# Optimization experiments

Hardware: AMD Instinct MI355X
Metric: run time of the kernel (lower is better)

The kernel has to match this reference:

```python
import jax, jax.numpy as jnp
import numpy as np

NUM_CLUSTERS = 16
HIDDEN = 1024
BOTTLENECK = 128
N_TOKENS = 65536


def setup_inputs() -> dict:
    key = jax.random.key(0)
    k_h, k_ids, k_w1, k_b1, k_w2, k_b2 = jax.random.split(key, 6)
    h = jax.random.normal(k_h, (N_TOKENS, HIDDEN), dtype=jnp.float32)
    cluster_ids = jax.random.randint(k_ids, (N_TOKENS,), 0, NUM_CLUSTERS)
    # Stacked per-cluster adapter params (torch Linear: y = x @ W.T + b; we store
    # already-transposed weights so forward is x @ W1[c]).
    s1 = 1.0 / np.sqrt(HIDDEN)
    s2 = 1.0 / np.sqrt(BOTTLENECK)
    W1 = jax.random.uniform(k_w1, (NUM_CLUSTERS, HIDDEN, BOTTLENECK), jnp.float32, -s1, s1)
    b1 = jax.random.uniform(k_b1, (NUM_CLUSTERS, BOTTLENECK), jnp.float32, -s1, s1)
    # Original inits these to zero; use small random values so grads are non-trivial.
    W2 = jax.random.uniform(k_w2, (NUM_CLUSTERS, BOTTLENECK, HIDDEN), jnp.float32, -s2, s2) * 0.02
    b2 = jax.random.uniform(k_b2, (NUM_CLUSTERS, HIDDEN), jnp.float32, -s2, s2) * 0.02
    return {"h": h, "cluster_ids": cluster_ids, "W1": W1, "b1": b1, "W2": W2, "b2": b2}


def reference(h, cluster_ids, W1, b1, W2, b2):
    # h: [N, H]; cluster_ids: [N]; W1: [K, H, B]; b1: [K, B]; W2: [K, B, H]; b2: [K, H]
    # out[n] = h[n] + adapter_{cluster_ids[n]}(h[n])
    K = W1.shape[0]
    out = jnp.zeros_like(h)
    for c in range(K):  # fixed small expert count; select per-token result via where
        mid = jax.nn.gelu(h @ W1[c] + b1[c], approximate=False)  # [N, B]
        y = h + mid @ W2[c] + b2[c]                               # [N, H]
        out = jnp.where((cluster_ids == c)[:, None], y, out)
    return out
```

## Files before the change

kernel.cpp:

```cpp
#include <hip/hip_runtime.h>
#include <hip/hip_bf16.h>
#include <math.h>

#define NUM_CLUSTERS 16
#define HIDDEN 1024
#define BOT 128
#define NTOK 65536

typedef __attribute__((ext_vector_type(8))) short bf16x8;
typedef __attribute__((ext_vector_type(4))) float f32x4;

typedef __attribute__((address_space(3))) unsigned int lds_u32;
typedef const __attribute__((address_space(1))) unsigned int glb_u32;

__device__ __forceinline__ void gload16(const void* g, void* l) {
  __builtin_amdgcn_global_load_lds((glb_u32*)g, (lds_u32*)l, 16, 0, 0);
}

__device__ __forceinline__ unsigned short f2bf(float x) {
  union { float f; unsigned u; } v; v.f = x;
  unsigned r = v.u + 0x7fffu + ((v.u >> 16) & 1u);
  return (unsigned short)(r >> 16);
}

__device__ __forceinline__ bf16x8 pack8(float4 a, float4 b) {
  bf16x8 r;
  r[0] = (short)f2bf(a.x); r[1] = (short)f2bf(a.y);
  r[2] = (short)f2bf(a.z); r[3] = (short)f2bf(a.w);
  r[4] = (short)f2bf(b.x); r[5] = (short)f2bf(b.y);
  r[6] = (short)f2bf(b.z); r[7] = (short)f2bf(b.w);
  return r;
}

#define SWZS(row, sidx) ((sidx) ^ (((row) & 7) << 3))
#define SW4(row, fidx) ((fidx) ^ (((row) & 7) << 2))

#define SCB() __builtin_amdgcn_sched_barrier(0)
#define VMW(n)                                          \
  do {                                                  \
    SCB();                                              \
    asm volatile("s_waitcnt vmcnt(" #n ")" ::: "memory"); \
    SCB();                                              \
  } while (0)
#define SBAR()                                  \
  do {                                          \
    SCB();                                      \
    __builtin_amdgcn_s_barrier();               \
    SCB();                                      \
  } while (0)
#define LGKM0() asm volatile("s_waitcnt lgkmcnt(0)" ::: "memory")

__device__ __forceinline__ int xcd_swz(int bid, int nwg) {
  const int nx = 8;
  int q = nwg / nx, r = nwg % nx;
  int xcd = bid % nx, idx = bid / nx;
  int b = (xcd < r) ? xcd * (q + 1) : r * (q + 1) + (xcd - r) * q;
  return b + idx;
}


__global__ void k_zero(int* p) {
  if (threadIdx.x < 64) p[threadIdx.x] = 0;
}

__global__ void k_hist(const int* __restrict__ ids, int* __restrict__ counts) {
  __shared__ int lh[NUM_CLUSTERS];
  if (threadIdx.x < NUM_CLUSTERS) lh[threadIdx.x] = 0;
  __syncthreads();
  int i = blockIdx.x * blockDim.x + threadIdx.x;
  int stride = gridDim.x * blockDim.x;
  for (; i < NTOK; i += stride) atomicAdd(&lh[ids[i]], 1);
  __syncthreads();
  if (threadIdx.x < NUM_CLUSTERS) atomicAdd(&counts[threadIdx.x], lh[threadIdx.x]);
}

__global__ void k_scan(const int* __restrict__ counts, int* __restrict__ offsets,
                       int* __restrict__ cursor) {
  if (threadIdx.x == 0 && blockIdx.x == 0) {
    int s = 0;
    for (int c = 0; c < NUM_CLUSTERS; ++c) {
      offsets[c] = s; cursor[c] = s; s += counts[c];
    }
    offsets[NUM_CLUSTERS] = s;
  }
}

__global__ void k_scatter(const int* __restrict__ ids, int* cursor,
                          int* __restrict__ perm) {
  __shared__ int lh[NUM_CLUSTERS], lbase[NUM_CLUSTERS];
  const int tid = threadIdx.x;
  if (tid < NUM_CLUSTERS) lh[tid] = 0;
  __syncthreads();
  const int i = blockIdx.x * 256 + tid;
  const int cc = ids[i];
  const int r = atomicAdd(&lh[cc], 1);
  __syncthreads();
  if (tid < NUM_CLUSTERS) lbase[tid] = atomicAdd(&cursor[tid], lh[tid]);
  __syncthreads();
  perm[lbase[cc] + r] = i;
}

__global__ void k_w1til(const float* __restrict__ W1, unsigned short* __restrict__ outw) {
  const int id = blockIdx.x * 256 + threadIdx.x;
  const int c  = id >> 14;
  const int ks = (id >> 10) & 15;
  const int q  = id & 1023;
  const int o  = q << 4;
  const int row = o >> 7;
  const int lb  = (o & 127) ^ ((row & 7) << 4);
  const int k0  = ks * 64 + (lb >> 1);
  const float* src = W1 + ((size_t)c * HIDDEN + k0) * BOT + row;
  unsigned short v[8];
  #pragma unroll
  for (int j = 0; j < 8; ++j) v[j] = f2bf(src[(size_t)j * BOT]);
  *(uint4*)((char*)outw + ((size_t)(c * 16 + ks)) * 16384 + o) = *(const uint4*)v;
}

__global__ void k_w2lin(const float* __restrict__ W2, unsigned short* __restrict__ outw) {
  const int id = blockIdx.x * 256 + threadIdx.x;
  const int c   = id >> 14;
  const int rem = id & 16383;
  const int fg  = rem >> 6;
  const int l   = rem & 63;
  const int nc  = fg >> 4, kk = (fg >> 2) & 3, nf = fg & 3;
  const int n   = nc * 64 + nf * 16 + (l & 15);
  const int k0  = kk * 32 + (l >> 4) * 8;
  const float* src = W2 + ((size_t)c * BOT + k0) * HIDDEN + n;
  unsigned short v[8];
  #pragma unroll
  for (int j = 0; j < 8; ++j) v[j] = f2bf(src[(size_t)j * HIDDEN]);
  *(uint4*)(outw + (size_t)id * 8) = *(const uint4*)v;
}

__global__ void k_w2til(const float* __restrict__ W2, unsigned short* __restrict__ outw) {
  const int id = blockIdx.x * 256 + threadIdx.x;
  const int c  = id >> 14;
  const int nc = (id >> 10) & 15;
  const int q  = id & 1023;
  const int o  = q << 4;
  const int row = o >> 8;
  const int lb  = (o & 255) ^ ((row & 7) << 4);
  const int b0  = lb >> 1;
  const int n   = nc * 64 + row;
  const float* src = W2 + ((size_t)c * BOT + b0) * HIDDEN + n;
  unsigned short v[8];
  #pragma unroll
  for (int j = 0; j < 8; ++j) v[j] = f2bf(src[(size_t)j * HIDDEN]);
  *(uint4*)((char*)outw + ((size_t)(c * 16 + nc)) * 16384 + o) = *(const uint4*)v;
}

__device__ __forceinline__ bool locate(const int* offsets, int bid, int TMv,
                                       int& c, int& base, int& nvalid) {
  int t = bid;
  for (c = 0; c < NUM_CLUSTERS; ++c) {
    int cnt = offsets[c + 1] - offsets[c];
    int nt = (cnt + TMv - 1) / TMv;
    if (t < nt) {
      base = offsets[c] + t * TMv;
      nvalid = min(TMv, offsets[c + 1] - base);
      return true;
    }
    t -= nt;
  }
  return false;
}

__global__ __launch_bounds__(512, 6) void k_gemm1(
    const float* __restrict__ h, const float* __restrict__ b1g,
    const unsigned short* __restrict__ W1til, const int* __restrict__ offsets,
    const int* __restrict__ perm, unsigned short* __restrict__ midg) {

  __shared__ __align__(16) unsigned short sA[2][4096];
  __shared__ __align__(16) unsigned short sB[2][8192];
  __shared__ int sTok[64];

  const int tid = threadIdx.x;
  const int l = tid & 63, w = tid >> 6;
  const int lr = l & 15, lg = l >> 4;
  const int wr = w >> 2, wc = w & 3;
  const int row = tid >> 3, o8 = tid & 7;

  const int nwg = NTOK / 64 + NUM_CLUSTERS;
  int c, base, nvalid;
  if (!locate(offsets, xcd_swz(blockIdx.x, nwg), 64, c, base, nvalid)) return;

  if (tid < 64) sTok[tid] = perm[base + min(tid, nvalid - 1)];
  LGKM0();
  SBAR();

  const unsigned short* w1base = W1til + (size_t)c * 16 * 8192;
  const float* hrow = h + (long)sTok[row] * HIDDEN + o8 * 8;

  float4 vaA[2], vaB[2];
  vaA[0] = *(const float4*)(hrow);       vaA[1] = *(const float4*)(hrow + 4);
  SCB();
  gload16(w1base + tid * 8, &sB[0][tid * 8]);
  gload16(w1base + 4096 + tid * 8, &sB[0][4096 + tid * 8]);
  SCB();
  vaB[0] = *(const float4*)(hrow + 64);  vaB[1] = *(const float4*)(hrow + 68);
  SCB();
  *(bf16x8*)&sA[0][SWZS(row, row * 64 + o8 * 8)] = pack8(vaA[0], vaA[1]);
  LGKM0();
  VMW(2);
  SBAR();

  f32x4 acc[2][2];
  #pragma unroll
  for (int i = 0; i < 2; ++i)
    #pragma unroll
    for (int j = 0; j < 2; ++j) { f32x4 z = {0.f, 0.f, 0.f, 0.f}; acc[i][j] = z; }

#define G1_MFMA(CUR)                                                          \
  do {                                                                        \
    _Pragma("unroll")                                                         \
    for (int kk = 0; kk < 2; ++kk) {                                          \
      bf16x8 af[2], bfr[2];                                                   \
      _Pragma("unroll")                                                       \
      for (int mf = 0; mf < 2; ++mf) {                                        \
        const int m = wr * 32 + mf * 16 + lr;                                 \
        af[mf] = *(const bf16x8*)&sA[CUR][SWZS(m, m * 64 + kk * 32 + lg * 8)];\
      }                                                                       \
      _Pragma("unroll")                                                       \
      for (int nf = 0; nf < 2; ++nf) {                                        \
        const int rn = wc * 32 + nf * 16 + lr;                                \
        bfr[nf] = *(const bf16x8*)&sB[CUR][SWZS(rn, rn * 64 + kk * 32 + lg * 8)]; \
      }                                                                       \
      _Pragma("unroll")                                                       \
      for (int mf = 0; mf < 2; ++mf)                                          \
        _Pragma("unroll")                                                     \
        for (int nf = 0; nf < 2; ++nf)                                        \
          acc[mf][nf] = __builtin_amdgcn_mfma_f32_16x16x32_bf16(              \
              af[mf], bfr[nf], acc[mf][nf], 0, 0, 0);                         \
    }                                                                         \
  } while (0)

  #pragma unroll
  for (int t = 0; t < 16; ++t) {
    const int cur = t & 1;
    if (t < 15) {
      const unsigned short* w1s = w1base + (t + 1) * 8192;
      gload16(w1s + tid * 8, &sB[cur ^ 1][tid * 8]);
      gload16(w1s + 4096 + tid * 8, &sB[cur ^ 1][4096 + tid * 8]);
      SCB();
    }
    if (t < 14) {
      if (t & 1) {
        vaB[0] = *(const float4*)(hrow + (t + 2) * 64);
        vaB[1] = *(const float4*)(hrow + (t + 2) * 64 + 4);
      } else {
        vaA[0] = *(const float4*)(hrow + (t + 2) * 64);
        vaA[1] = *(const float4*)(hrow + (t + 2) * 64 + 4);
      }
      SCB();
    }
    G1_MFMA(cur);
    if (t < 15) {
      const float4* src = ((t + 1) & 1) ? vaB : vaA;
      *(bf16x8*)&sA[cur ^ 1][SWZS(row, row * 64 + o8 * 8)] = pack8(src[0], src[1]);
      if (t < 14) { VMW(2); } else { VMW(0); }
      LGKM0();
      SBAR();
    }
  }
#undef G1_MFMA

  float b1v[2];
  #pragma unroll
  for (int nf = 0; nf < 2; ++nf) b1v[nf] = b1g[c * BOT + wc * 32 + nf * 16 + lr];
  #pragma unroll
  for (int mf = 0; mf < 2; ++mf) {
    #pragma unroll
    for (int nf = 0; nf < 2; ++nf) {
      #pragma unroll
      for (int r = 0; r < 4; ++r) {
        float x = acc[mf][nf][r] + b1v[nf];
        float g = 0.5f * x * (1.0f + erff(x * 0.70710678118654752f));
        const int m = wr * 32 + mf * 16 + lg * 4 + r;
        if (m < nvalid) {
          const int n = wc * 32 + nf * 16 + lr;
          midg[(size_t)(base + m) * BOT + n] = f2bf(g);
        }
      }
    }
  }
}


__global__ __launch_bounds__(512, 6) void k_gemm2(
    const float* __restrict__ h, const float* __restrict__ b2g,
    const unsigned short* __restrict__ W2lin, const int* __restrict__ offsets,
    const int* __restrict__ perm, const unsigned short* __restrict__ midg,
    float* __restrict__ out) {

  __shared__ __align__(16) unsigned short sB[2][8192];
  __shared__ __align__(16) float sOut[8 * 512];
  __shared__ int sTok[64];

  const int tid = threadIdx.x;
  const int l = tid & 63, w = tid >> 6;
  const int lr = l & 15, lg = l >> 4;
  const int wrow = (w & 3) * 16;
  const int ch = w >> 2;

  const int nwg = NTOK / 64 + NUM_CLUSTERS;
  int c, base, nvalid;
  if (!locate(offsets, xcd_swz(blockIdx.x, nwg), 64, c, base, nvalid)) return;

  if (tid < 64) sTok[tid] = perm[base + min(tid, nvalid - 1)];
  __syncthreads();

  const unsigned short* wlin = W2lin + (size_t)c * 131072;

  const long amrow = (long)(base + min(wrow + lr, nvalid - 1)) * BOT;
  bf16x8 ma[4];
  #pragma unroll
  for (int kk = 0; kk < 4; ++kk)
    ma[kk] = *(const bf16x8*)(midg + amrow + kk * 32 + lg * 8);

  const int er = l >> 2, ecq = l & 3;
  const long etok = (long)sTok[wrow + er] * HIDDEN;
  const float* hrow = h + etok;
  float* orow = out + etok;
  float* sW = sOut + w * 512;
  const float* b2c = b2g + c * HIDDEN;
  const int ecol = ch * 32 + ecq * 8;

  gload16(wlin + tid * 8, &sB[0][tid * 8]);
  gload16(wlin + 4096 + tid * 8, &sB[0][4096 + tid * 8]);
  VMW(0);
  SBAR();

  for (int nc = 0; nc < 16; ++nc) {
    const int cur = nc & 1;
    float4 hv0 = *(const float4*)(hrow + nc * 64 + ecol);
    float4 hv1 = *(const float4*)(hrow + nc * 64 + ecol + 4);
    float4 bv0 = *(const float4*)(b2c + nc * 64 + ecol);
    float4 bv1 = *(const float4*)(b2c + nc * 64 + ecol + 4);
    SCB();
    if (nc < 15) {
      const unsigned short* ws2 = wlin + (nc + 1) * 8192;
      gload16(ws2 + tid * 8, &sB[cur ^ 1][tid * 8]);
      gload16(ws2 + 4096 + tid * 8, &sB[cur ^ 1][4096 + tid * 8]);
      SCB();
    }

    f32x4 acc[2];
    { f32x4 z = {0.f, 0.f, 0.f, 0.f}; acc[0] = z; acc[1] = z; }
    #pragma unroll
    for (int kk = 0; kk < 4; ++kk) {
      #pragma unroll
      for (int nf = 0; nf < 2; ++nf) {
        const bf16x8 bf =
            *(const bf16x8*)&sB[cur][(kk * 4 + ch * 2 + nf) * 512 + l * 8];
        acc[nf] = __builtin_amdgcn_mfma_f32_16x16x32_bf16(ma[kk], bf, acc[nf], 0, 0, 0);
      }
    }

    #pragma unroll
    for (int nf = 0; nf < 2; ++nf) {
      #pragma unroll
      for (int r = 0; r < 4; ++r) {
        const int m = lg * 4 + r;
        const int n = nf * 16 + lr;
        sW[(m * 32 + n) ^ ((m & 7) << 2)] = acc[nf][r];
      }
    }
    {
      const int fb = er * 32 + ecq * 8;
      const float4 y0 = *(const float4*)&sW[(fb) ^ ((er & 7) << 2)];
      const float4 y1 = *(const float4*)&sW[(fb + 4) ^ ((er & 7) << 2)];
      float4 o0, o1;
      o0.x = y0.x + hv0.x + bv0.x; o0.y = y0.y + hv0.y + bv0.y;
      o0.z = y0.z + hv0.z + bv0.z; o0.w = y0.w + hv0.w + bv0.w;
      o1.x = y1.x + hv1.x + bv1.x; o1.y = y1.y + hv1.y + bv1.y;
      o1.z = y1.z + hv1.z + bv1.z; o1.w = y1.w + hv1.w + bv1.w;
      *(float4*)(orow + nc * 64 + ecol)     = o0;
      *(float4*)(orow + nc * 64 + ecol + 4) = o1;
    }
    if (nc < 15) {
      VMW(2);
      SBAR();
    }
  }
}

#define FSWZ(row, sidx) ((sidx) ^ (((row) & 7) << 3))

__global__ __launch_bounds__(256, 2) void k_fused(
    const float* __restrict__ h, const float* __restrict__ b1g,
    const float* __restrict__ b2g, const unsigned short* __restrict__ W1til,
    const unsigned short* __restrict__ W2til, const int* __restrict__ offsets,
    const int* __restrict__ perm, float* __restrict__ out) {

  __shared__ __align__(16) unsigned short sAB[16384];
  __shared__ __align__(16) unsigned short sMid[16384];
  __shared__ int sTok[128];

  const int tid = threadIdx.x;
  const int l = tid & 63, w = tid >> 6;
  const int wr = w >> 1, wc = w & 1;
  const int lr = l & 15, lg = l >> 4;

  int c, base, nvalid;
  if (!locate(offsets, blockIdx.x, 128, c, base, nvalid)) return;

  if (tid < 128) sTok[tid] = perm[base + min(tid, nvalid - 1)];
  __syncthreads();

  const unsigned short* w1base = W1til + (size_t)c * 16 * 8192;
  const unsigned short* w2base = W2til + (size_t)c * 16 * 8192;

  const int arow = tid >> 1, ahalf = tid & 1;
  const long htok = (long)sTok[arow] * HIDDEN;

  f32x4 acc[4][4];
  #pragma unroll
  for (int i = 0; i < 4; ++i)
    #pragma unroll
    for (int j = 0; j < 4; ++j) { f32x4 z = {0.f, 0.f, 0.f, 0.f}; acc[i][j] = z; }

  for (int ks = 0; ks < 16; ++ks) {
    __syncthreads();
    const unsigned short* w1s = w1base + ks * 8192;
    #pragma unroll
    for (int j = 0; j < 4; ++j)
      gload16(w1s + j * 2048 + tid * 8, &sAB[8192 + j * 2048 + tid * 8]);
    {
      const float* hp = h + htok + ks * 64 + ahalf * 32;
      float4 v0 = *(const float4*)(hp + 0),  v1 = *(const float4*)(hp + 4);
      float4 v2 = *(const float4*)(hp + 8),  v3 = *(const float4*)(hp + 12);
      float4 v4 = *(const float4*)(hp + 16), v5 = *(const float4*)(hp + 20);
      float4 v6 = *(const float4*)(hp + 24), v7 = *(const float4*)(hp + 28);
      const int sb = arow * 64 + ahalf * 32;
      *(bf16x8*)&sAB[FSWZ(arow, sb + 0)]  = pack8(v0, v1);
      *(bf16x8*)&sAB[FSWZ(arow, sb + 8)]  = pack8(v2, v3);
      *(bf16x8*)&sAB[FSWZ(arow, sb + 16)] = pack8(v4, v5);
      *(bf16x8*)&sAB[FSWZ(arow, sb + 24)] = pack8(v6, v7);
    }
    __syncthreads();
    #pragma unroll
    for (int kk = 0; kk < 2; ++kk) {
      bf16x8 af[4], bfr[4];
      #pragma unroll
      for (int mf = 0; mf < 4; ++mf) {
        const int rw = wr * 64 + mf * 16 + lr;
        af[mf] = *(const bf16x8*)&sAB[FSWZ(rw, rw * 64 + kk * 32 + lg * 8)];
      }
      #pragma unroll
      for (int nf = 0; nf < 4; ++nf) {
        const int rn = wc * 64 + nf * 16 + lr;
        bfr[nf] = *(const bf16x8*)&sAB[8192 + FSWZ(rn, rn * 64 + kk * 32 + lg * 8)];
      }
      #pragma unroll
      for (int mf = 0; mf < 4; ++mf)
        #pragma unroll
        for (int nf = 0; nf < 4; ++nf)
          acc[mf][nf] = __builtin_amdgcn_mfma_f32_16x16x32_bf16(af[mf], bfr[nf], acc[mf][nf], 0, 0, 0);
    }
  }

  float b1v[4];
  #pragma unroll
  for (int nf = 0; nf < 4; ++nf) b1v[nf] = b1g[c * BOT + wc * 64 + nf * 16 + lr];
  #pragma unroll
  for (int mf = 0; mf < 4; ++mf)
    #pragma unroll
    for (int nf = 0; nf < 4; ++nf)
      #pragma unroll
      for (int r = 0; r < 4; ++r) {
        float x = acc[mf][nf][r] + b1v[nf];
        float g = 0.5f * x * (1.0f + erff(x * 0.70710678118654752f));
        const int m = wr * 64 + mf * 16 + lg * 4 + r;
        const int n = wc * 64 + nf * 16 + lr;
        sMid[FSWZ(m, m * 128 + n)] = f2bf(g);
      }

  for (int nc = 0; nc < 16; ++nc) {
    __syncthreads();
    #pragma unroll
    for (int j = 0; j < 4; ++j)
      gload16(w2base + nc * 8192 + j * 2048 + tid * 8, &sAB[j * 2048 + tid * 8]);
    __syncthreads();

    f32x4 a2[4][2];
    #pragma unroll
    for (int i = 0; i < 4; ++i)
      #pragma unroll
      for (int j = 0; j < 2; ++j) { f32x4 z = {0.f, 0.f, 0.f, 0.f}; a2[i][j] = z; }

    #pragma unroll
    for (int kk = 0; kk < 4; ++kk) {
      bf16x8 af[4], bfr[2];
      #pragma unroll
      for (int mf = 0; mf < 4; ++mf) {
        const int m = wr * 64 + mf * 16 + lr;
        af[mf] = *(const bf16x8*)&sMid[FSWZ(m, m * 128 + kk * 32 + lg * 8)];
      }
      #pragma unroll
      for (int nf = 0; nf < 2; ++nf) {
        const int rn = wc * 32 + nf * 16 + lr;
        bfr[nf] = *(const bf16x8*)&sAB[FSWZ(rn, rn * 128 + kk * 32 + lg * 8)];
      }
      #pragma unroll
      for (int mf = 0; mf < 4; ++mf)
        #pragma unroll
        for (int nf = 0; nf < 2; ++nf)
          a2[mf][nf] = __builtin_amdgcn_mfma_f32_16x16x32_bf16(af[mf], bfr[nf], a2[mf][nf], 0, 0, 0);
    }

    #pragma unroll
    for (int nf = 0; nf < 2; ++nf) {
      const int nn = nc * 64 + wc * 32 + nf * 16 + lr;
      const float b2v = b2g[c * HIDDEN + nn];
      #pragma unroll
      for (int mf = 0; mf < 4; ++mf)
        #pragma unroll
        for (int r = 0; r < 4; ++r) {
          const int m = wr * 64 + mf * 16 + lg * 4 + r;
          if (m < nvalid) {
            const long tk = (long)sTok[m] * HIDDEN;
            out[tk + nn] = h[tk + nn] + a2[mf][nf][r] + b2v;
          }
        }
    }
  }
}

extern "C" void kernel_launch(void* const* d_in, const int* in_sizes, int n_in,
                              void* d_out, int out_size, void* d_ws, size_t ws_size,
                              hipStream_t stream) {
  const float* h   = (const float*)d_in[0];
  const int*   ids = (const int*)d_in[1];
  const float* W1  = (const float*)d_in[2];
  const float* b1  = (const float*)d_in[3];
  const float* W2  = (const float*)d_in[4];
  const float* b2  = (const float*)d_in[5];
  float* out = (float*)d_out;

  char* ws = (char*)d_ws;
  int* counts  = (int*)ws;
  int* cursor  = (int*)(ws + 64);
  int* offsets = (int*)(ws + 128);
  int* perm    = (int*)(ws + 256);
  unsigned short* W1til = (unsigned short*)(ws + 262400);
  unsigned short* W2buf = W1til + (size_t)16 * 16 * 8192;
  unsigned short* midg  = W2buf + (size_t)16 * 16 * 8192;
  const size_t need = 262400 + 2 * (size_t)16 * 16 * 8192 * 2 +
                      (size_t)NTOK * BOT * 2;

  k_zero<<<1, 64, 0, stream>>>(counts);
  k_hist<<<256, 256, 0, stream>>>(ids, counts);
  k_scan<<<1, 64, 0, stream>>>(counts, offsets, cursor);
  k_scatter<<<NTOK / 256, 256, 0, stream>>>(ids, cursor, perm);
  k_w1til<<<1024, 256, 0, stream>>>(W1, W1til);

  if (ws_size >= need) {
    k_w2lin<<<1024, 256, 0, stream>>>(W2, W2buf);
    const int nwg = NTOK / 64 + NUM_CLUSTERS;
    k_gemm1<<<nwg, 512, 0, stream>>>(h, b1, W1til, offsets, perm, midg);
    k_gemm2<<<nwg, 512, 0, stream>>>(h, b2, W2buf, offsets, perm, midg, out);
  } else {
    k_w2til<<<1024, 256, 0, stream>>>(W2, W2buf);
    k_fused<<<NTOK / 128 + NUM_CLUSTERS, 256, 0, stream>>>(
        h, b1, b2, W1til, W2buf, offsets, perm, out);
  }
}
```

Measured before the change: 268.5 us.

## Fuse adapter GEMM1 and GEMM2 into one kernel with mid kept in LDS

Merges the two grouped GEMM kernels into one, so the GELU bottleneck activations are written to LDS instead of a global bf16 buffer and read back directly as MFMA A-operands. This removes the global round trip of the mid tensor and one kernel launch. The epilogue now writes output straight from MFMA accumulator layout with scalar loads and stores instead of staging through LDS for float4 stores, which may make h loads and output stores less coalesced. Out-of-range rows in partial tiles also write duplicates of the last valid token.

```diff
diff --git a/kernel.cpp b/kernel.cpp
--- a/kernel.cpp
+++ b/kernel.cpp
@@ -33,7 +33,6 @@
 }
 
 #define SWZS(row, sidx) ((sidx) ^ (((row) & 7) << 3))
-#define SW4(row, fidx) ((fidx) ^ (((row) & 7) << 2))
 
 #define SCB() __builtin_amdgcn_sched_barrier(0)
 #define VMW(n)                                          \
@@ -165,10 +164,12 @@
   return false;
 }
 
-__global__ __launch_bounds__(512, 6) void k_gemm1(
+
+__global__ __launch_bounds__(512, 6) void k_fuse(
     const float* __restrict__ h, const float* __restrict__ b1g,
-    const unsigned short* __restrict__ W1til, const int* __restrict__ offsets,
-    const int* __restrict__ perm, unsigned short* __restrict__ midg) {
+    const float* __restrict__ b2g, const unsigned short* __restrict__ W1til,
+    const unsigned short* __restrict__ W2lin, const int* __restrict__ offsets,
+    const int* __restrict__ perm, float* __restrict__ out) {
 
   __shared__ __align__(16) unsigned short sA[2][4096];
   __shared__ __align__(16) unsigned short sB[2][8192];
@@ -189,6 +190,7 @@
   SBAR();
 
   const unsigned short* w1base = W1til + (size_t)c * 16 * 8192;
+  const unsigned short* wlin   = W2lin + (size_t)c * 131072;
   const float* hrow = h + (long)sTok[row] * HIDDEN + o8 * 8;
 
   float4 vaA[2], vaB[2];
@@ -264,78 +266,67 @@
   }
 #undef G1_MFMA
 
-  float b1v[2];
-  #pragma unroll
-  for (int nf = 0; nf < 2; ++nf) b1v[nf] = b1g[c * BOT + wc * 32 + nf * 16 + lr];
-  #pragma unroll
-  for (int mf = 0; mf < 2; ++mf) {
-    #pragma unroll
-    for (int nf = 0; nf < 2; ++nf) {
-      #pragma unroll
-      for (int r = 0; r < 4; ++r) {
-        float x = acc[mf][nf][r] + b1v[nf];
-        float g = 0.5f * x * (1.0f + erff(x * 0.70710678118654752f));
-        const int m = wr * 32 + mf * 16 + lg * 4 + r;
-        if (m < nvalid) {
+  unsigned short* sMid = &sA[0][0];
+  gload16(wlin + tid * 8, &sB[0][tid * 8]);
+  gload16(wlin + 4096 + tid * 8, &sB[0][4096 + tid * 8]);
+  SCB();
+  SBAR();
+
+  {
+    float b1v[2];
+    #pragma unroll
+    for (int nf = 0; nf < 2; ++nf) b1v[nf] = b1g[c * BOT + wc * 32 + nf * 16 + lr];
+    #pragma unroll
+    for (int mf = 0; mf < 2; ++mf) {
+      #pragma unroll
+      for (int nf = 0; nf < 2; ++nf) {
+        #pragma unroll
+        for (int r = 0; r < 4; ++r) {
+          float x = acc[mf][nf][r] + b1v[nf];
+          float g = 0.5f * x * (1.0f + erff(x * 0.70710678118654752f));
+          const int m = wr * 32 + mf * 16 + lg * 4 + r;
           const int n = wc * 32 + nf * 16 + lr;
-          midg[(size_t)(base + m) * BOT + n] = f2bf(g);
+          sMid[SWZS(m, m * 128 + n)] = f2bf(g);
         }
       }
     }
   }
-}
-
-
-__global__ __launch_bounds__(512, 6) void k_gemm2(
-    const float* __restrict__ h, const float* __restrict__ b2g,
-    const unsigned short* __restrict__ W2lin, const int* __restrict__ offsets,
-    const int* __restrict__ perm, const unsigned short* __restrict__ midg,
-    float* __restrict__ out) {
-
-  __shared__ __align__(16) unsigned short sB[2][8192];
-  __shared__ __align__(16) float sOut[8 * 512];
-  __shared__ int sTok[64];
-
-  const int tid = threadIdx.x;
-  const int l = tid & 63, w = tid >> 6;
-  const int lr = l & 15, lg = l >> 4;
+  LGKM0();
+  VMW(0);
+  SBAR();
+
   const int wrow = (w & 3) * 16;
   const int ch = w >> 2;
 
-  const int nwg = NTOK / 64 + NUM_CLUSTERS;
-  int c, base, nvalid;
-  if (!locate(offsets, xcd_swz(blockIdx.x, nwg), 64, c, base, nvalid)) return;
-
-  if (tid < 64) sTok[tid] = perm[base + min(tid, nvalid - 1)];
-  __syncthreads();
-
-  const unsigned short* wlin = W2lin + (size_t)c * 131072;
-
-  const long amrow = (long)(base + min(wrow + lr, nvalid - 1)) * BOT;
   bf16x8 ma[4];
-  #pragma unroll
-  for (int kk = 0; kk < 4; ++kk)
-    ma[kk] = *(const bf16x8*)(midg + amrow + kk * 32 + lg * 8);
-
-  const int er = l >> 2, ecq = l & 3;
-  const long etok = (long)sTok[wrow + er] * HIDDEN;
-  const float* hrow = h + etok;
-  float* orow = out + etok;
-  float* sW = sOut + w * 512;
+  {
+    const int mrow = wrow + lr;
+    #pragma unroll
+    for (int kk = 0; kk < 4; ++kk)
+      ma[kk] = *(const bf16x8*)&sMid[SWZS(mrow, mrow * 128 + kk * 32 + lg * 8)];
+  }
+
+  const float* hr[4];
+  float* orp[4];
+  #pragma unroll
+  for (int r = 0; r < 4; ++r) {
+    const long tk = (long)sTok[wrow + lg * 4 + r] * HIDDEN;
+    hr[r] = h + tk;
+    orp[r] = out + tk;
+  }
   const float* b2c = b2g + c * HIDDEN;
-  const int ecol = ch * 32 + ecq * 8;
-
-  gload16(wlin + tid * 8, &sB[0][tid * 8]);
-  gload16(wlin + 4096 + tid * 8, &sB[0][4096 + tid * 8]);
-  VMW(0);
-  SBAR();
 
   for (int nc = 0; nc < 16; ++nc) {
     const int cur = nc & 1;
-    float4 hv0 = *(const float4*)(hrow + nc * 64 + ecol);
-    float4 hv1 = *(const float4*)(hrow + nc * 64 + ecol + 4);
-    float4 bv0 = *(const float4*)(b2c + nc * 64 + ecol);
-    float4 bv1 = *(const float4*)(b2c + nc * 64 + ecol + 4);
+    const int cb = nc * 64 + ch * 32;
+    float hv[2][4], bv[2];
+    #pragma unroll
+    for (int nf = 0; nf < 2; ++nf)
+      #pragma unroll
+      for (int r = 0; r < 4; ++r)
+        hv[nf][r] = hr[r][cb + nf * 16 + lr];
+    #pragma unroll
+    for (int nf = 0; nf < 2; ++nf) bv[nf] = b2c[cb + nf * 16 + lr];
     SCB();
     if (nc < 15) {
       const unsigned short* ws2 = wlin + (nc + 1) * 8192;
@@ -344,15 +335,15 @@
       SCB();
     }
 
-    f32x4 acc[2];
-    { f32x4 z = {0.f, 0.f, 0.f, 0.f}; acc[0] = z; acc[1] = z; }
+    f32x4 a2[2];
+    { f32x4 z = {0.f, 0.f, 0.f, 0.f}; a2[0] = z; a2[1] = z; }
     #pragma unroll
     for (int kk = 0; kk < 4; ++kk) {
       #pragma unroll
       for (int nf = 0; nf < 2; ++nf) {
         const bf16x8 bf =
             *(const bf16x8*)&sB[cur][(kk * 4 + ch * 2 + nf) * 512 + l * 8];
-        acc[nf] = __builtin_amdgcn_mfma_f32_16x16x32_bf16(ma[kk], bf, acc[nf], 0, 0, 0);
+        a2[nf] = __builtin_amdgcn_mfma_f32_16x16x32_bf16(ma[kk], bf, a2[nf], 0, 0, 0);
       }
     }
 
@@ -360,25 +351,11 @@
     for (int nf = 0; nf < 2; ++nf) {
       #pragma unroll
       for (int r = 0; r < 4; ++r) {
-        const int m = lg * 4 + r;
-        const int n = nf * 16 + lr;
-        sW[(m * 32 + n) ^ ((m & 7) << 2)] = acc[nf][r];
-      }
-    }
-    {
-      const int fb = er * 32 + ecq * 8;
-      const float4 y0 = *(const float4*)&sW[(fb) ^ ((er & 7) << 2)];
-      const float4 y1 = *(const float4*)&sW[(fb + 4) ^ ((er & 7) << 2)];
-      float4 o0, o1;
-      o0.x = y0.x + hv0.x + bv0.x; o0.y = y0.y + hv0.y + bv0.y;
-      o0.z = y0.z + hv0.z + bv0.z; o0.w = y0.w + hv0.w + bv0.w;
-      o1.x = y1.x + hv1.x + bv1.x; o1.y = y1.y + hv1.y + bv1.y;
-      o1.z = y1.z + hv1.z + bv1.z; o1.w = y1.w + hv1.w + bv1.w;
-      *(float4*)(orow + nc * 64 + ecol)     = o0;
-      *(float4*)(orow + nc * 64 + ecol + 4) = o1;
+        orp[r][cb + nf * 16 + lr] = a2[nf][r] + hv[nf][r] + bv[nf];
+      }
     }
     if (nc < 15) {
-      VMW(2);
+      VMW(8);
       SBAR();
     }
   }
@@ -544,9 +521,7 @@
   int* perm    = (int*)(ws + 256);
   unsigned short* W1til = (unsigned short*)(ws + 262400);
   unsigned short* W2buf = W1til + (size_t)16 * 16 * 8192;
-  unsigned short* midg  = W2buf + (size_t)16 * 16 * 8192;
-  const size_t need = 262400 + 2 * (size_t)16 * 16 * 8192 * 2 +
-                      (size_t)NTOK * BOT * 2;
+  const size_t need = 262400 + 2 * (size_t)16 * 16 * 8192 * 2;
 
   k_zero<<<1, 64, 0, stream>>>(counts);
   k_hist<<<256, 256, 0, stream>>>(ids, counts);
@@ -557,8 +532,7 @@
   if (ws_size >= need) {
     k_w2lin<<<1024, 256, 0, stream>>>(W2, W2buf);
     const int nwg = NTOK / 64 + NUM_CLUSTERS;
-    k_gemm1<<<nwg, 512, 0, stream>>>(h, b1, W1til, offsets, perm, midg);
-    k_gemm2<<<nwg, 512, 0, stream>>>(h, b2, W2buf, offsets, perm, midg, out);
+    k_fuse<<<nwg, 512, 0, stream>>>(h, b1, b2, W1til, W2buf, offsets, perm, out);
   } else {
     k_w2til<<<1024, 256, 0, stream>>>(W2, W2buf);
     k_fused<<<NTOK / 128 + NUM_CLUSTERS, 256, 0, stream>>>(
```

After: 244.3 us. 9.0% less time.
